# Kernel optimization log

Measured on AMD Instinct MI355X. Metric: run time of the kernel, lower is better.

Reference implementation:

```python
import jax, jax.numpy as jnp
import numpy as np

N, E = 50000, 800000
NODE_DIM, EDGE_DIM = 128, 32
EGO_H, PEER_H, EDGE_H = 64, 64, 32  # node_hidden=128 split; edge_hidden=32


def setup_inputs() -> dict:
    key = jax.random.key(0)
    ks = jax.random.split(key, 9)
    x = jax.random.normal(ks[0], (N, NODE_DIM), dtype=jnp.float32)
    edge_attrs = jax.random.normal(ks[1], (E, EDGE_DIM), dtype=jnp.float32)
    edge_index = jax.random.randint(ks[2], (2, E), 0, N, dtype=jnp.int32)
    # Linear params (torch convention: W [out, in]), num_layers=1 -> single emb Linear per MLPLayer
    def lin(k, out_d, in_d):
        kw, kb = jax.random.split(k)
        s = 1.0 / np.sqrt(in_d)
        return (jax.random.uniform(kw, (out_d, in_d), minval=-s, maxval=s, dtype=jnp.float32),
                jax.random.uniform(kb, (out_d,), minval=-s, maxval=s, dtype=jnp.float32))
    W_peer, b_peer = lin(ks[3], PEER_H + EDGE_H, NODE_DIM + EDGE_DIM)
    W_ego, b_ego = lin(ks[4], EGO_H, NODE_DIM)
    W_edge, b_edge = lin(ks[5], EDGE_H, EDGE_DIM)
    return {"x": x, "edge_attrs": edge_attrs,
            "W_peer": W_peer, "b_peer": b_peer,
            "W_ego": W_ego, "b_ego": b_ego,
            "W_edge": W_edge, "b_edge": b_edge,
            "edge_index": edge_index}


def reference(x, edge_attrs, W_peer, b_peer, W_ego, b_ego, W_edge, b_edge, edge_index):
    n = x.shape[0]
    # adj_t = SparseTensor(row=ei[0], col=ei[1]).t() -> row = ei[1], col = ei[0]
    row = edge_index[1]
    col = edge_index[0]

    # ego branch
    h_ego = jax.nn.relu(x @ W_ego.T + b_ego)  # [N, EGO_H]

    # degree-based row normalization: deg^-0.5 per adj_t row, inf -> 0
    deg = jax.ops.segment_sum(jnp.ones((row.shape[0],), x.dtype), row, num_segments=n)
    dinv = jnp.where(deg > 0, jax.lax.rsqrt(jnp.maximum(deg, 1.0)) * (deg > 0), 0.0)
    dinv = jnp.where(deg > 0, deg ** -0.5, 0.0)
    norm_val = dinv[row]  # [E]

    # peer branch: gather x[row], cat edge_attrs, linear, normalize, scatter-sum over row
    peer_features = jnp.concatenate([x[row], edge_attrs], axis=1)  # [E, NODE_DIM+EDGE_DIM]
    peer_msg = norm_val[:, None] * (peer_features @ W_peer.T + b_peer)
    h_peer = jax.nn.relu(jax.ops.segment_sum(peer_msg, row, num_segments=n))  # [N, PEER_H+EDGE_H]

    # edge branch
    h_e = jax.nn.relu(edge_attrs @ W_edge.T + b_edge)  # [E, EDGE_H]
    h_e_agg = jax.ops.segment_sum(h_e, row, num_segments=n)  # adj_t.set_value(h_edge).sum(1)
    # norm.matmul(h_edge): out[i] = sum_{e: row[e]==i} norm_val[e] * h_e_agg[col[e]]
    h_e_mm = jax.ops.segment_sum(norm_val[:, None] * h_e_agg[col], row, num_segments=n)
    h_edge = jnp.concatenate([h_e_agg, h_e_mm], axis=1)  # [N, 2*EDGE_H]

    out = jnp.concatenate([h_ego, h_edge, h_peer], axis=1)  # [N, 224]
    return out
```

## Files before the change

### kernel.cpp

```cpp
#include <hip/hip_runtime.h>


typedef float f32x4 __attribute__((ext_vector_type(4)));
typedef short bf16x8 __attribute__((ext_vector_type(8)));

#define BP 256

__device__ __forceinline__ unsigned short f2bf(float f) {
    unsigned u = __float_as_uint(f);
    u += 0x7fffu + ((u >> 16) & 1u);
    return (unsigned short)(u >> 16);
}
__device__ __forceinline__ float bf2f(unsigned short u) {
    return __uint_as_float((unsigned)u << 16);
}
__device__ __forceinline__ ushort4 pk4(float4 v) {
    return (ushort4){f2bf(v.x), f2bf(v.y), f2bf(v.z), f2bf(v.w)};
}
__device__ __forceinline__ bf16x8 pack8(float4 lo, float4 hi) {
    bf16x8 r;
    r[0]=(short)f2bf(lo.x); r[1]=(short)f2bf(lo.y); r[2]=(short)f2bf(lo.z); r[3]=(short)f2bf(lo.w);
    r[4]=(short)f2bf(hi.x); r[5]=(short)f2bf(hi.y); r[6]=(short)f2bf(hi.z); r[7]=(short)f2bf(hi.w);
    return r;
}
__device__ __forceinline__ bf16x8 ld_bfrag(const unsigned short* bp) {
    ushort4 lo = *reinterpret_cast<const ushort4*>(bp);
    ushort4 hi = *reinterpret_cast<const ushort4*>(bp + 16);
    bf16x8 b;
    b[0]=(short)lo.x; b[1]=(short)lo.y; b[2]=(short)lo.z; b[3]=(short)lo.w;
    b[4]=(short)hi.x; b[5]=(short)hi.y; b[6]=(short)hi.z; b[7]=(short)hi.w;
    return b;
}

__global__ __launch_bounds__(256) void k_zero(int* __restrict__ deg, int N) {
    int i = blockIdx.x * blockDim.x + threadIdx.x;
    if (i < N) deg[i] = 0;
}

__global__ __launch_bounds__(256) void k_hist(const int* __restrict__ row,
                                              int* __restrict__ deg, int E) {
    int e = blockIdx.x * blockDim.x + threadIdx.x;
    if (e < E) atomicAdd(&deg[row[e]], 1);
}

__global__ __launch_bounds__(256) void k_scan_partial(const int* __restrict__ deg,
                                                      int* __restrict__ bsum, int N) {
    __shared__ int sh[256];
    int base = blockIdx.x * 1024 + threadIdx.x * 4;
    int s = 0;
#pragma unroll
    for (int q = 0; q < 4; ++q) { int i = base + q; if (i < N) s += deg[i]; }
    sh[threadIdx.x] = s;
    __syncthreads();
    for (int off = 128; off > 0; off >>= 1) {
        if (threadIdx.x < off) sh[threadIdx.x] += sh[threadIdx.x + off];
        __syncthreads();
    }
    if (threadIdx.x == 0) bsum[blockIdx.x] = sh[0];
}

__global__ void k_scan_mid(const int* __restrict__ bsum, int* __restrict__ boff,
                           int* __restrict__ off, int NB, int N) {
    if (threadIdx.x == 0 && blockIdx.x == 0) {
        int acc = 0;
        for (int b = 0; b < NB; ++b) { boff[b] = acc; acc += bsum[b]; }
        off[N] = acc;
    }
}

__global__ __launch_bounds__(256) void k_scan_final(
    const int* __restrict__ deg, const int* __restrict__ boff,
    int* __restrict__ off, int* __restrict__ cursor,
    float* __restrict__ sd, float* __restrict__ rdeg, int* __restrict__ nstart,
    float* __restrict__ eagg, float* __restrict__ sea, int N)
{
    __shared__ int sh[256];
    int t = threadIdx.x;
    int base = blockIdx.x * 1024 + t * 4;
    int v[4];
#pragma unroll
    for (int q = 0; q < 4; ++q) v[q] = (base + q < N) ? deg[base + q] : 0;
    int ts = v[0] + v[1] + v[2] + v[3];
    sh[t] = ts;
    __syncthreads();
    int incl = ts;
    for (int d = 1; d < 256; d <<= 1) {
        int val = (t >= d) ? sh[t - d] : 0;
        __syncthreads();
        incl += val;
        sh[t] = incl;
        __syncthreads();
    }
    int running = boff[blockIdx.x] + incl - ts;
#pragma unroll
    for (int q = 0; q < 4; ++q) {
        int i = base + q;
        if (i < N) {
            int s = running, e = running + v[q];
            off[i] = s; cursor[i] = s;
            int dg = v[q];
            sd[i]   = dg > 0 ? sqrtf((float)dg) : 0.f;
            rdeg[i] = dg > 0 ? 1.f / (float)dg : 0.f;
            for (int b = (s + BP - 1) / BP; b * BP < e; ++b) nstart[b] = i;
            bool zneed = (dg == 0) || ((s / BP) != ((e - 1) / BP));
            if (zneed) {
                float4 z = {0.f, 0.f, 0.f, 0.f};
                float4* pe = reinterpret_cast<float4*>(eagg + (size_t)i * 32);
                float4* ps = reinterpret_cast<float4*>(sea  + (size_t)i * 32);
#pragma unroll
                for (int q2 = 0; q2 < 8; ++q2) { pe[q2] = z; ps[q2] = z; }
            }
            running = e;
        }
    }
}

__global__ __launch_bounds__(256) void k_scatter(const int* __restrict__ row,
                                                 const int* __restrict__ col,
                                                 int* __restrict__ cursor,
                                                 int2* __restrict__ edat, int E) {
    int e = blockIdx.x * blockDim.x + threadIdx.x;
    if (e >= E) return;
    int pos = atomicAdd(&cursor[row[e]], 1);
    edat[pos] = make_int2(e, col[e]);
}

__global__ __launch_bounds__(256) void k_prepw(const float* __restrict__ W_ego,
                                               const float* __restrict__ W_peer,
                                               const float* __restrict__ W_edge,
                                               unsigned short* __restrict__ Bt,
                                               unsigned short* __restrict__ Bte) {
    int idx = blockIdx.x * blockDim.x + threadIdx.x;
    if (idx < 160 * 160) {
        int n = idx / 160, k = idx % 160;
        float v;
        if (n < 64) v = (k < 128) ? W_ego[n * 128 + k] : 0.f;
        else        v = W_peer[(n - 64) * 160 + k];
        Bt[idx] = f2bf(v);
    } else if (idx < 160 * 160 + 32 * 32) {
        int j = idx - 160 * 160;
        Bte[j] = f2bf(W_edge[j]);
    }
}

__global__ __launch_bounds__(512) void k_fused(
    const float* __restrict__ ea, const int2* __restrict__ edat,
    const int* __restrict__ off, const int* __restrict__ nstart,
    const unsigned short* __restrict__ Bte, const float* __restrict__ b_edge,
    float* __restrict__ eagg, float* __restrict__ sea, int N, int E)
{
    __shared__ unsigned short hs [BP][36];
    __shared__ unsigned short asr[BP][36];
    const int tid  = threadIdx.x;
    const int w    = tid >> 6;
    const int lane = tid & 63;
    const int n16  = lane & 15;
    const int h    = lane >> 4;
    const int P    = blockIdx.x * BP;

    {
        const int tA = w * 32 + n16;
        const int p0 = min(P + tA,      E - 1);
        const int p1 = min(P + tA + 16, E - 1);
        const int e0i = edat[p0].x;
        const int e1i = edat[p1].x;
        const float* ap0 = ea + (size_t)e0i * 32 + h * 4;
        const float* ap1 = ea + (size_t)e1i * 32 + h * 4;
        float4 lo0 = *reinterpret_cast<const float4*>(ap0);
        float4 hi0 = *reinterpret_cast<const float4*>(ap0 + 16);
        float4 lo1 = *reinterpret_cast<const float4*>(ap1);
        float4 hi1 = *reinterpret_cast<const float4*>(ap1 + 16);

        *reinterpret_cast<ushort4*>(&asr[tA][h * 4])           = pk4(lo0);
        *reinterpret_cast<ushort4*>(&asr[tA][16 + h * 4])      = pk4(hi0);
        *reinterpret_cast<ushort4*>(&asr[tA + 16][h * 4])      = pk4(lo1);
        *reinterpret_cast<ushort4*>(&asr[tA + 16][16 + h * 4]) = pk4(hi1);

        bf16x8 a0 = pack8(lo0, hi0);
        bf16x8 a1 = pack8(lo1, hi1);
        bf16x8 b0 = ld_bfrag(Bte + (size_t)n16 * 32 + h * 4);
        bf16x8 b1 = ld_bfrag(Bte + (size_t)(16 + n16) * 32 + h * 4);
        f32x4 d00 = {0.f,0.f,0.f,0.f}, d01 = {0.f,0.f,0.f,0.f};
        f32x4 d10 = {0.f,0.f,0.f,0.f}, d11 = {0.f,0.f,0.f,0.f};
        d00 = __builtin_amdgcn_mfma_f32_16x16x32_bf16(a0, b0, d00, 0, 0, 0);
        d01 = __builtin_amdgcn_mfma_f32_16x16x32_bf16(a0, b1, d01, 0, 0, 0);
        d10 = __builtin_amdgcn_mfma_f32_16x16x32_bf16(a1, b0, d10, 0, 0, 0);
        d11 = __builtin_amdgcn_mfma_f32_16x16x32_bf16(a1, b1, d11, 0, 0, 0);

        const int tr0 = w * 32 + h * 4;
        float be0 = b_edge[n16], be1 = b_edge[16 + n16];
#pragma unroll
        for (int r = 0; r < 4; ++r) {
            hs[tr0 + r][n16]           = f2bf(fmaxf(d00[r] + be0, 0.f));
            hs[tr0 + r][16 + n16]      = f2bf(fmaxf(d01[r] + be1, 0.f));
            hs[tr0 + 16 + r][n16]      = f2bf(fmaxf(d10[r] + be0, 0.f));
            hs[tr0 + 16 + r][16 + n16] = f2bf(fmaxf(d11[r] + be1, 0.f));
        }
    }
    __syncthreads();

    const int c = lane & 7, sub = lane >> 3;
    const int node0 = nstart[blockIdx.x];

    for (int n = node0 + w; n < N; n += 8) {
        int s0 = off[n];
        if (s0 >= P + BP) break;
        int e0 = off[n + 1];
        int s = max(s0, P) - P, eEnd = min(e0, P + BP) - P;
        float4 hv = {0.f,0.f,0.f,0.f}, av = {0.f,0.f,0.f,0.f};
        for (int t = s + sub; t < eEnd; t += 8) {
            ushort4 uh = *reinterpret_cast<const ushort4*>(&hs [t][c * 4]);
            ushort4 ua = *reinterpret_cast<const ushort4*>(&asr[t][c * 4]);
            hv.x += bf2f(uh.x); hv.y += bf2f(uh.y); hv.z += bf2f(uh.z); hv.w += bf2f(uh.w);
            av.x += bf2f(ua.x); av.y += bf2f(ua.y); av.z += bf2f(ua.z); av.w += bf2f(ua.w);
        }
#pragma unroll
        for (int m = 8; m < 64; m <<= 1) {
            hv.x += __shfl_xor(hv.x, m); hv.y += __shfl_xor(hv.y, m);
            hv.z += __shfl_xor(hv.z, m); hv.w += __shfl_xor(hv.w, m);
            av.x += __shfl_xor(av.x, m); av.y += __shfl_xor(av.y, m);
            av.z += __shfl_xor(av.z, m); av.w += __shfl_xor(av.w, m);
        }
        if (lane < 8) {
            float* pe = eagg + (size_t)n * 32 + c * 4;
            float* ps = sea  + (size_t)n * 32 + c * 4;
            bool interior = (s0 >= P) && (e0 <= P + BP);
            if (interior) {
                *reinterpret_cast<float4*>(pe) = hv;
                *reinterpret_cast<float4*>(ps) = av;
            } else {
                atomicAdd(pe+0,hv.x); atomicAdd(pe+1,hv.y);
                atomicAdd(pe+2,hv.z); atomicAdd(pe+3,hv.w);
                atomicAdd(ps+0,av.x); atomicAdd(ps+1,av.y);
                atomicAdd(ps+2,av.z); atomicAdd(ps+3,av.w);
            }
        }
    }
}

__global__ __launch_bounds__(256) void k_mmagg(
    const int2* __restrict__ edat, const int* __restrict__ off,
    const float* __restrict__ eagg, float* __restrict__ out, int N)
{
    int wid  = (blockIdx.x * blockDim.x + threadIdx.x) >> 6;
    int lane = threadIdx.x & 63;
    if (wid >= N) return;
    int s = off[wid], e = off[wid + 1];
    int c   = lane & 7;
    int sub = lane >> 3;
    float4 acc = {0.f, 0.f, 0.f, 0.f};
    float4 acc2 = {0.f, 0.f, 0.f, 0.f};
    for (int t0 = s; t0 < e; t0 += 16) {
        int t1 = t0 + sub, t2 = t0 + 8 + sub;
        if (t1 < e) {
            float4 v = reinterpret_cast<const float4*>(eagg + (size_t)edat[t1].y * 32)[c];
            acc.x += v.x; acc.y += v.y; acc.z += v.z; acc.w += v.w;
        }
        if (t2 < e) {
            float4 v = reinterpret_cast<const float4*>(eagg + (size_t)edat[t2].y * 32)[c];
            acc2.x += v.x; acc2.y += v.y; acc2.z += v.z; acc2.w += v.w;
        }
    }
    acc.x += acc2.x; acc.y += acc2.y; acc.z += acc2.z; acc.w += acc2.w;
#pragma unroll
    for (int m = 8; m < 64; m <<= 1) {
        acc.x += __shfl_xor(acc.x, m);
        acc.y += __shfl_xor(acc.y, m);
        acc.z += __shfl_xor(acc.z, m);
        acc.w += __shfl_xor(acc.w, m);
    }
    int dg = e - s;
    float dinv = dg > 0 ? rsqrtf((float)dg) : 0.f;
    if (lane < 8) {
        float4 o4 = {acc.x * dinv, acc.y * dinv, acc.z * dinv, acc.w * dinv};
        reinterpret_cast<float4*>(out + (size_t)wid * 224 + 96)[c] = o4;
        float4 eg = reinterpret_cast<const float4*>(eagg + (size_t)wid * 32)[c];
        reinterpret_cast<float4*>(out + (size_t)wid * 224 + 64)[c] = eg;
    }
}

__global__ __launch_bounds__(256) void k_node3(
    const float* __restrict__ x, const float* __restrict__ sea,
    const float* __restrict__ sd, const float* __restrict__ rdeg,
    const unsigned short* __restrict__ Bt,
    const float* __restrict__ b_ego, const float* __restrict__ b_peer,
    float* __restrict__ out, int N)
{
    const int lane = threadIdx.x & 63;
    const int wv   = threadIdx.x >> 6;
    const int wm   = blockIdx.x * 64 + wv * 16;
    const int n16  = lane & 15;
    const int h    = lane >> 4;

    const int m_l = min(wm + n16, N - 1);

    f32x4 acc[10];
#pragma unroll
    for (int f = 0; f < 10; ++f) acc[f] = (f32x4){0.f,0.f,0.f,0.f};

#pragma unroll
    for (int kc = 0; kc < 5; ++kc) {
        bf16x8 bfr[10];
#pragma unroll
        for (int f = 0; f < 10; ++f)
            bfr[f] = ld_bfrag(Bt + (size_t)(f * 16 + n16) * 160 + kc * 32 + h * 4);
        float4 lo, hi;
        if (kc < 4) {
            const float* ap = x + (size_t)m_l * 128 + kc * 32 + h * 4;
            lo = *reinterpret_cast<const float4*>(ap);
            hi = *reinterpret_cast<const float4*>(ap + 16);
        } else {
            float r = rdeg[m_l];
            const float* ap = sea + (size_t)m_l * 32 + h * 4;
            lo = *reinterpret_cast<const float4*>(ap);
            hi = *reinterpret_cast<const float4*>(ap + 16);
            lo.x*=r; lo.y*=r; lo.z*=r; lo.w*=r;
            hi.x*=r; hi.y*=r; hi.z*=r; hi.w*=r;
        }
        bf16x8 a = pack8(lo, hi);
#pragma unroll
        for (int f = 0; f < 10; ++f)
            acc[f] = __builtin_amdgcn_mfma_f32_16x16x32_bf16(a, bfr[f], acc[f], 0, 0, 0);
    }

    const int r4 = h * 4;
    float sdv[4];
#pragma unroll
    for (int r = 0; r < 4; ++r) {
        int node = wm + r4 + r;
        sdv[r] = (node < N) ? sd[node] : 0.f;
    }
#pragma unroll
    for (int f = 0; f < 10; ++f) {
        int c = f * 16 + n16;
        float be = (c < 64)  ? b_ego[c] : 0.f;
        float bp = (c >= 64) ? b_peer[c - 64] : 0.f;
#pragma unroll
        for (int r = 0; r < 4; ++r) {
            int node = wm + r4 + r;
            if (node >= N) continue;
            float v = acc[f][r];
            if (c < 64)
                out[(size_t)node * 224 + c] = fmaxf(v + be, 0.f);
            else
                out[(size_t)node * 224 + 64 + c] = fmaxf(sdv[r] * (v + bp), 0.f);
        }
    }
}

extern "C" void kernel_launch(void* const* d_in, const int* in_sizes, int n_in,
                              void* d_out, int out_size, void* d_ws, size_t ws_size,
                              hipStream_t stream)
{
    const float* x      = (const float*)d_in[0];
    const float* ea     = (const float*)d_in[1];
    const float* W_peer = (const float*)d_in[2];
    const float* b_peer = (const float*)d_in[3];
    const float* W_ego  = (const float*)d_in[4];
    const float* b_ego  = (const float*)d_in[5];
    const float* W_edge = (const float*)d_in[6];
    const float* b_edge = (const float*)d_in[7];
    const int*   ei     = (const int*)d_in[8];

    const int N = in_sizes[0] / 128;
    const int E = in_sizes[8] / 2;
    const int* col = ei;
    const int* row = ei + E;
    const int nblocks = (E + BP - 1) / BP;

    int2*  edat    = (int2*)d_ws;
    int*   deg_i   = (int*)(edat + E);
    float* eagg    = (float*)(deg_i + N);
    float* sea     = eagg + (size_t)32 * N;
    int*   off     = (int*)(sea + (size_t)32 * N);
    int*   cursor  = off + (N + 1);
    int*   bsum    = cursor + N;
    int*   boff    = bsum + 64;
    float* sd      = (float*)(boff + 64);
    float* rdeg    = sd + N;
    int*   nstart  = (int*)(rdeg + N);
    unsigned short* Bt  = (unsigned short*)(nstart + nblocks);
    unsigned short* Bte = Bt + 160 * 160;
    float* out     = (float*)d_out;

    const int TB = 256;
    const int NB = (N + 1023) / 1024;
    k_zero        <<<(N + TB - 1) / TB, TB, 0, stream>>>(deg_i, N);
    k_prepw       <<<(160*160 + 32*32 + TB - 1) / TB, TB, 0, stream>>>(W_ego, W_peer, W_edge, Bt, Bte);
    k_hist        <<<(E + TB - 1) / TB, TB, 0, stream>>>(row, deg_i, E);
    k_scan_partial<<<NB, TB, 0, stream>>>(deg_i, bsum, N);
    k_scan_mid    <<<1, 64, 0, stream>>>(bsum, boff, off, NB, N);
    k_scan_final  <<<NB, TB, 0, stream>>>(deg_i, boff, off, cursor, sd, rdeg,
                                          nstart, eagg, sea, N);
    k_scatter     <<<(E + TB - 1) / TB, TB, 0, stream>>>(row, col, cursor, edat, E);

    k_fused<<<nblocks, 512, 0, stream>>>(ea, edat, off, nstart, Bte, b_edge,
                                         eagg, sea, N, E);

    const int agg_grid = (N + 3) / 4;
    k_mmagg<<<agg_grid, TB, 0, stream>>>(edat, off, eagg, out, N);
    k_node3<<<(N + 63) / 64, TB, 0, stream>>>(x, sea, sd, rdeg, Bt,
                                              b_ego, b_peer, out, N);
}
```

Measured before the change: 212.5 us.

## Pre-sort edge attributes to bf16 in CSR order using atomic ranks from histogram

The histogram kernel now records each edge's atomic rank, so the scatter no longer needs a second atomic cursor pass. The scatter kernel converts each edge's fp32 attributes to bf16 and writes them contiguously in CSR order, along with a sorted column array. The fused aggregation kernel and the mm-aggregation kernel then read contiguous bf16 rows and plain column indices instead of doing an indirect gather of fp32 rows through the edge-index pair. The trade-off is an extra write and read of a 64-byte-per-edge sorted buffer plus a rank array, in exchange for removing the random fp32 gather and one atomic pass.

Result: faster. 202.9 us (-4.5%).

```diff
diff --git a/kernel.cpp b/kernel.cpp
--- a/kernel.cpp
+++ b/kernel.cpp
@@ -3,6 +3,7 @@
 
 typedef float f32x4 __attribute__((ext_vector_type(4)));
 typedef short bf16x8 __attribute__((ext_vector_type(8)));
+typedef unsigned short u16x8 __attribute__((ext_vector_type(8)));
 
 #define BP 256
 
@@ -14,23 +15,22 @@
 __device__ __forceinline__ float bf2f(unsigned short u) {
     return __uint_as_float((unsigned)u << 16);
 }
-__device__ __forceinline__ ushort4 pk4(float4 v) {
-    return (ushort4){f2bf(v.x), f2bf(v.y), f2bf(v.z), f2bf(v.w)};
-}
-__device__ __forceinline__ bf16x8 pack8(float4 lo, float4 hi) {
-    bf16x8 r;
-    r[0]=(short)f2bf(lo.x); r[1]=(short)f2bf(lo.y); r[2]=(short)f2bf(lo.z); r[3]=(short)f2bf(lo.w);
-    r[4]=(short)f2bf(hi.x); r[5]=(short)f2bf(hi.y); r[6]=(short)f2bf(hi.z); r[7]=(short)f2bf(hi.w);
+__device__ __forceinline__ u16x8 pk8u(float4 lo, float4 hi) {
+    u16x8 r;
+    r[0]=f2bf(lo.x); r[1]=f2bf(lo.y); r[2]=f2bf(lo.z); r[3]=f2bf(lo.w);
+    r[4]=f2bf(hi.x); r[5]=f2bf(hi.y); r[6]=f2bf(hi.z); r[7]=f2bf(hi.w);
     return r;
 }
-__device__ __forceinline__ bf16x8 ld_bfrag(const unsigned short* bp) {
-    ushort4 lo = *reinterpret_cast<const ushort4*>(bp);
-    ushort4 hi = *reinterpret_cast<const ushort4*>(bp + 16);
+__device__ __forceinline__ bf16x8 mk_frag(ushort4 lo, ushort4 hi) {
     bf16x8 b;
     b[0]=(short)lo.x; b[1]=(short)lo.y; b[2]=(short)lo.z; b[3]=(short)lo.w;
     b[4]=(short)hi.x; b[5]=(short)hi.y; b[6]=(short)hi.z; b[7]=(short)hi.w;
     return b;
 }
+__device__ __forceinline__ bf16x8 ld_bfrag(const unsigned short* bp) {
+    return mk_frag(*reinterpret_cast<const ushort4*>(bp),
+                   *reinterpret_cast<const ushort4*>(bp + 16));
+}
 
 __global__ __launch_bounds__(256) void k_zero(int* __restrict__ deg, int N) {
     int i = blockIdx.x * blockDim.x + threadIdx.x;
@@ -38,9 +38,10 @@
 }
 
 __global__ __launch_bounds__(256) void k_hist(const int* __restrict__ row,
-                                              int* __restrict__ deg, int E) {
+                                              int* __restrict__ deg,
+                                              int* __restrict__ rank, int E) {
     int e = blockIdx.x * blockDim.x + threadIdx.x;
-    if (e < E) atomicAdd(&deg[row[e]], 1);
+    if (e < E) rank[e] = atomicAdd(&deg[row[e]], 1);
 }
 
 __global__ __launch_bounds__(256) void k_scan_partial(const int* __restrict__ deg,
@@ -70,7 +71,7 @@
 
 __global__ __launch_bounds__(256) void k_scan_final(
     const int* __restrict__ deg, const int* __restrict__ boff,
-    int* __restrict__ off, int* __restrict__ cursor,
+    int* __restrict__ off,
     float* __restrict__ sd, float* __restrict__ rdeg, int* __restrict__ nstart,
     float* __restrict__ eagg, float* __restrict__ sea, int N)
 {
@@ -97,7 +98,7 @@
         int i = base + q;
         if (i < N) {
             int s = running, e = running + v[q];
-            off[i] = s; cursor[i] = s;
+            off[i] = s;
             int dg = v[q];
             sd[i]   = dg > 0 ? sqrtf((float)dg) : 0.f;
             rdeg[i] = dg > 0 ? 1.f / (float)dg : 0.f;
@@ -115,14 +116,21 @@
     }
 }
 
-__global__ __launch_bounds__(256) void k_scatter(const int* __restrict__ row,
-                                                 const int* __restrict__ col,
-                                                 int* __restrict__ cursor,
-                                                 int2* __restrict__ edat, int E) {
+__global__ __launch_bounds__(256) void k_scatcvt(
+    const float* __restrict__ ea, const int* __restrict__ row,
+    const int* __restrict__ col, const int* __restrict__ off,
+    const int* __restrict__ rank,
+    unsigned short* __restrict__ easorted, int* __restrict__ colsort, int E)
+{
     int e = blockIdx.x * blockDim.x + threadIdx.x;
     if (e >= E) return;
-    int pos = atomicAdd(&cursor[row[e]], 1);
-    edat[pos] = make_int2(e, col[e]);
+    int pos = off[row[e]] + rank[e];
+    const float4* src = reinterpret_cast<const float4*>(ea + (size_t)e * 32);
+    u16x8* dst = reinterpret_cast<u16x8*>(easorted + (size_t)pos * 32);
+#pragma unroll
+    for (int q = 0; q < 4; ++q)
+        dst[q] = pk8u(src[2 * q], src[2 * q + 1]);
+    colsort[pos] = col[e];
 }
 
 __global__ __launch_bounds__(256) void k_prepw(const float* __restrict__ W_ego,
@@ -143,8 +151,8 @@
     }
 }
 
-__global__ __launch_bounds__(512) void k_fused(
-    const float* __restrict__ ea, const int2* __restrict__ edat,
+__global__ __launch_bounds__(512) void k_agg(
+    const unsigned short* __restrict__ easorted,
     const int* __restrict__ off, const int* __restrict__ nstart,
     const unsigned short* __restrict__ Bte, const float* __restrict__ b_edge,
     float* __restrict__ eagg, float* __restrict__ sea, int N, int E)
@@ -162,22 +170,20 @@
         const int tA = w * 32 + n16;
         const int p0 = min(P + tA,      E - 1);
         const int p1 = min(P + tA + 16, E - 1);
-        const int e0i = edat[p0].x;
-        const int e1i = edat[p1].x;
-        const float* ap0 = ea + (size_t)e0i * 32 + h * 4;
-        const float* ap1 = ea + (size_t)e1i * 32 + h * 4;
-        float4 lo0 = *reinterpret_cast<const float4*>(ap0);
-        float4 hi0 = *reinterpret_cast<const float4*>(ap0 + 16);
-        float4 lo1 = *reinterpret_cast<const float4*>(ap1);
-        float4 hi1 = *reinterpret_cast<const float4*>(ap1 + 16);
-
-        *reinterpret_cast<ushort4*>(&asr[tA][h * 4])           = pk4(lo0);
-        *reinterpret_cast<ushort4*>(&asr[tA][16 + h * 4])      = pk4(hi0);
-        *reinterpret_cast<ushort4*>(&asr[tA + 16][h * 4])      = pk4(lo1);
-        *reinterpret_cast<ushort4*>(&asr[tA + 16][16 + h * 4]) = pk4(hi1);
-
-        bf16x8 a0 = pack8(lo0, hi0);
-        bf16x8 a1 = pack8(lo1, hi1);
+        const unsigned short* r0 = easorted + (size_t)p0 * 32 + h * 4;
+        const unsigned short* r1 = easorted + (size_t)p1 * 32 + h * 4;
+        ushort4 lo0 = *reinterpret_cast<const ushort4*>(r0);
+        ushort4 hi0 = *reinterpret_cast<const ushort4*>(r0 + 16);
+        ushort4 lo1 = *reinterpret_cast<const ushort4*>(r1);
+        ushort4 hi1 = *reinterpret_cast<const ushort4*>(r1 + 16);
+
+        *reinterpret_cast<ushort4*>(&asr[tA][h * 4])           = lo0;
+        *reinterpret_cast<ushort4*>(&asr[tA][16 + h * 4])      = hi0;
+        *reinterpret_cast<ushort4*>(&asr[tA + 16][h * 4])      = lo1;
+        *reinterpret_cast<ushort4*>(&asr[tA + 16][16 + h * 4]) = hi1;
+
+        bf16x8 a0 = mk_frag(lo0, hi0);
+        bf16x8 a1 = mk_frag(lo1, hi1);
         bf16x8 b0 = ld_bfrag(Bte + (size_t)n16 * 32 + h * 4);
         bf16x8 b1 = ld_bfrag(Bte + (size_t)(16 + n16) * 32 + h * 4);
         f32x4 d00 = {0.f,0.f,0.f,0.f}, d01 = {0.f,0.f,0.f,0.f};
@@ -239,7 +245,7 @@
 }
 
 __global__ __launch_bounds__(256) void k_mmagg(
-    const int2* __restrict__ edat, const int* __restrict__ off,
+    const int* __restrict__ colsort, const int* __restrict__ off,
     const float* __restrict__ eagg, float* __restrict__ out, int N)
 {
     int wid  = (blockIdx.x * blockDim.x + threadIdx.x) >> 6;
@@ -253,11 +259,11 @@
     for (int t0 = s; t0 < e; t0 += 16) {
         int t1 = t0 + sub, t2 = t0 + 8 + sub;
         if (t1 < e) {
-            float4 v = reinterpret_cast<const float4*>(eagg + (size_t)edat[t1].y * 32)[c];
+            float4 v = reinterpret_cast<const float4*>(eagg + (size_t)colsort[t1] * 32)[c];
             acc.x += v.x; acc.y += v.y; acc.z += v.z; acc.w += v.w;
         }
         if (t2 < e) {
-            float4 v = reinterpret_cast<const float4*>(eagg + (size_t)edat[t2].y * 32)[c];
+            float4 v = reinterpret_cast<const float4*>(eagg + (size_t)colsort[t2] * 32)[c];
             acc2.x += v.x; acc2.y += v.y; acc2.z += v.z; acc2.w += v.w;
         }
     }
@@ -317,7 +323,10 @@
             lo.x*=r; lo.y*=r; lo.z*=r; lo.w*=r;
             hi.x*=r; hi.y*=r; hi.z*=r; hi.w*=r;
         }
-        bf16x8 a = pack8(lo, hi);
+        u16x8 au = pk8u(lo, hi);
+        bf16x8 a;
+#pragma unroll
+        for (int q = 0; q < 8; ++q) a[q] = (short)au[q];
 #pragma unroll
         for (int f = 0; f < 10; ++f)
             acc[f] = __builtin_amdgcn_mfma_f32_16x16x32_bf16(a, bfr[f], acc[f], 0, 0, 0);
@@ -368,37 +377,39 @@
     const int* row = ei + E;
     const int nblocks = (E + BP - 1) / BP;
 
-    int2*  edat    = (int2*)d_ws;
-    int*   deg_i   = (int*)(edat + E);
-    float* eagg    = (float*)(deg_i + N);
-    float* sea     = eagg + (size_t)32 * N;
-    int*   off     = (int*)(sea + (size_t)32 * N);
-    int*   cursor  = off + (N + 1);
-    int*   bsum    = cursor + N;
-    int*   boff    = bsum + 64;
-    float* sd      = (float*)(boff + 64);
-    float* rdeg    = sd + N;
-    int*   nstart  = (int*)(rdeg + N);
-    unsigned short* Bt  = (unsigned short*)(nstart + nblocks);
-    unsigned short* Bte = Bt + 160 * 160;
-    float* out     = (float*)d_out;
+    int*            rank     = (int*)d_ws;
+    unsigned short* easorted = (unsigned short*)(rank + E);
+    int*            colsort  = (int*)(easorted + (size_t)32 * E);
+    int*            deg_i    = colsort + E;
+    float*          eagg     = (float*)(deg_i + N);
+    float*          sea      = eagg + (size_t)32 * N;
+    int*            off      = (int*)(sea + (size_t)32 * N);
+    int*            bsum     = off + (N + 1);
+    int*            boff     = bsum + 64;
+    float*          sd       = (float*)(boff + 64);
+    float*          rdeg     = sd + N;
+    int*            nstart   = (int*)(rdeg + N);
+    unsigned short* Bt       = (unsigned short*)(nstart + nblocks);
+    unsigned short* Bte      = Bt + 160 * 160;
+    float*          out      = (float*)d_out;
 
     const int TB = 256;
     const int NB = (N + 1023) / 1024;
     k_zero        <<<(N + TB - 1) / TB, TB, 0, stream>>>(deg_i, N);
     k_prepw       <<<(160*160 + 32*32 + TB - 1) / TB, TB, 0, stream>>>(W_ego, W_peer, W_edge, Bt, Bte);
-    k_hist        <<<(E + TB - 1) / TB, TB, 0, stream>>>(row, deg_i, E);
+    k_hist        <<<(E + TB - 1) / TB, TB, 0, stream>>>(row, deg_i, rank, E);
     k_scan_partial<<<NB, TB, 0, stream>>>(deg_i, bsum, N);
     k_scan_mid    <<<1, 64, 0, stream>>>(bsum, boff, off, NB, N);
-    k_scan_final  <<<NB, TB, 0, stream>>>(deg_i, boff, off, cursor, sd, rdeg,
+    k_scan_final  <<<NB, TB, 0, stream>>>(deg_i, boff, off, sd, rdeg,
                                           nstart, eagg, sea, N);
-    k_scatter     <<<(E + TB - 1) / TB, TB, 0, stream>>>(row, col, cursor, edat, E);
-
-    k_fused<<<nblocks, 512, 0, stream>>>(ea, edat, off, nstart, Bte, b_edge,
-                                         eagg, sea, N, E);
+    k_scatcvt     <<<(E + TB - 1) / TB, TB, 0, stream>>>(ea, row, col, off, rank,
+                                                         easorted, colsort, E);
+
+    k_agg<<<nblocks, 512, 0, stream>>>(easorted, off, nstart, Bte, b_edge,
+                                       eagg, sea, N, E);
 
     const int agg_grid = (N + 3) / 4;
-    k_mmagg<<<agg_grid, TB, 0, stream>>>(edat, off, eagg, out, N);
+    k_mmagg<<<agg_grid, TB, 0, stream>>>(colsort, off, eagg, out, N);
     k_node3<<<(N + 63) / 64, TB, 0, stream>>>(x, sea, sd, rdeg, Bt,
                                               b_ego, b_peer, out, N);
 }
```
